# Optimization experiments

Measured on AMD Instinct MI355X. Metric: run time of the kernel, lower is better.

## Reference

```python
import jax, jax.numpy as jnp
import numpy as np

B, L, C, NH = 512, 196, 384, 12
HW = 14  # window side

def _relative_position_index(h, w):
    coords = np.stack(np.meshgrid(np.arange(h), np.arange(w), indexing='ij'))  # [2,h,w]
    cf = coords.reshape(2, -1)                       # [2, L]
    rel = cf[:, :, None] - cf[:, None, :]            # [2, L, L]
    rel = rel.transpose(1, 2, 0).astype(np.int64)    # [L, L, 2]
    rel[..., 0] += h - 1
    rel[..., 1] += w - 1
    rel[..., 0] *= 2 * w - 1
    return rel.sum(-1)                               # [L, L]

def setup_inputs() -> dict:
    key = jax.random.key(0)
    ks = jax.random.split(key, 5)
    hd = C // NH
    x = jax.random.normal(ks[0], (B, L, C), dtype=jnp.float32)
    # weights stored as [in, out] (equivalent to torch Linear weight.T)
    qkv_w = jax.random.normal(ks[1], (C, 3 * C), dtype=jnp.float32) * (C ** -0.5)
    qkv_b = jnp.zeros((3 * C,), dtype=jnp.float32)
    proj_w = jax.random.normal(ks[2], (C, C), dtype=jnp.float32) * (C ** -0.5)
    proj_b = jnp.zeros((C,), dtype=jnp.float32)
    bias_table = jax.random.normal(ks[3], ((2 * HW - 1) ** 2, NH), dtype=jnp.float32) * 0.02
    rel_index = jnp.asarray(_relative_position_index(HW, HW), dtype=jnp.int32)
    return {"x": x, "qkv_w": qkv_w, "qkv_b": qkv_b, "proj_w": proj_w,
            "proj_b": proj_b, "bias_table": bias_table, "rel_index": rel_index}

def reference(x, qkv_w, qkv_b, proj_w, proj_b, bias_table, rel_index):
    b, l, c = x.shape
    nh = bias_table.shape[1]
    hd = c // nh
    scale = hd ** -0.5
    qkv = (x @ qkv_w + qkv_b).reshape(b, l, 3, nh, hd).transpose(2, 0, 3, 1, 4)  # [3,B,nh,L,hd]
    q, k, v = qkv[0] * scale, qkv[1], qkv[2]
    attn = jnp.einsum('bhqd,bhkd->bhqk', q, k)                 # [B,nh,L,L]
    bias = bias_table[rel_index]                               # [L,L,nh]
    attn = attn + bias.transpose(2, 0, 1)[None]                # add [1,nh,L,L]
    attn = jax.nn.softmax(attn, axis=-1)
    out = jnp.einsum('bhqk,bhkd->bhqd', attn, v)               # [B,nh,L,hd]
    out = out.transpose(0, 2, 1, 3).reshape(b, l, c)
    return out @ proj_w + proj_b
```

## Files before the change

### kernel.cpp

```cpp
#include <hip/hip_runtime.h>
#include <hip/hip_bf16.h>
#include <stdint.h>

typedef __hip_bfloat16 bf16;
typedef __attribute__((ext_vector_type(8))) short frag8;
typedef __attribute__((ext_vector_type(4))) float floatx4;

#define B_WIN 512
#define L_TOK 196
#define C_DIM 384
#define NH    12
#define HD    32
#define QP    208
#define KPAD  224
#define VSTR  236
#define QSCALE 0.2550348555f

#if defined(__has_builtin)
#if __has_builtin(__builtin_amdgcn_exp2f)
#define EXP2(x) __builtin_amdgcn_exp2f(x)
#endif
#endif
#ifndef EXP2
#define EXP2(x) exp2f(x)
#endif

__device__ __forceinline__ void async_cp16(const void* g, void* l) {
  __builtin_amdgcn_global_load_lds(
      (const __attribute__((address_space(1))) unsigned int*)g,
      (__attribute__((address_space(3))) unsigned int*)l, 16, 0, 0);
}

__device__ __forceinline__ unsigned short f2bf_bits(float f) {
  bf16 b = __float2bfloat16(f);
  return *(unsigned short*)&b;
}

__device__ __forceinline__ float bfu2f(short u) {
  union { uint32_t i; float f; } c;
  c.i = ((uint32_t)(unsigned short)u) << 16;
  return c.f;
}

__global__ void cast_to_bf16(const float* __restrict__ src, bf16* __restrict__ dst) {
  int i = blockIdx.x * 256 + threadIdx.x;
  float4 v = ((const float4*)src)[i];
  ushort4 o;
  o.x = f2bf_bits(v.x); o.y = f2bf_bits(v.y);
  o.z = f2bf_bits(v.z); o.w = f2bf_bits(v.w);
  ((ushort4*)dst)[i] = o;
}

__global__ void transpose_cast(const float* __restrict__ src, bf16* __restrict__ dst,
                               int K, int N) {
  int idx = blockIdx.x * 256 + threadIdx.x;
  if (idx >= K * N) return;
  int k = idx / N, n = idx - k * N;
  dst[n * K + k] = __float2bfloat16(src[idx]);
}

__global__ void bias_fill(const float* __restrict__ table, const int* __restrict__ rel,
                          bf16* __restrict__ biasb) {
  int idx = blockIdx.x * 256 + threadIdx.x;
  int h = idx / (QP * KPAD);
  int rem = idx - h * (QP * KPAD);
  int q = rem / KPAD, r2 = rem - q * KPAD;
  int kk = r2 >> 5, quad = (r2 >> 3) & 3, i = r2 & 7;
  int k = kk * 32 + quad * 8 + ((i >= 4) ? 4 : 0) + (i & 3);
  float v;
  if (q >= L_TOK)      v = 0.f;
  else if (k >= L_TOK) v = -1e30f;
  else                 v = table[rel[q * L_TOK + k] * NH + h] * 1.4426950408889634f;
  biasb[idx] = __float2bfloat16(v);
}

__device__ __forceinline__ void storev(bf16* p, float v)  { *p = __float2bfloat16(v); }
__device__ __forceinline__ void storev(float* p, float v) { *p = v; }

template <typename OT>
__global__ __launch_bounds__(256) void gemm_bt(
    const bf16* __restrict__ A, const bf16* __restrict__ Bt,
    const float* __restrict__ bias, OT* __restrict__ C,
    int M, int N, int K, int lda, int qcols, int nbn, int panel) {
  __shared__ __align__(16) bf16 sA[3][128 * 32];
  __shared__ __align__(16) bf16 sB[3][128 * 32];
  const int tid = threadIdx.x;
  const int wave = tid >> 6, lane = tid & 63;
  const int SUPER = panel * nbn;
  const int bid = blockIdx.x;
  const int sb = bid / SUPER, rsp = bid - sb * SUPER;
  const long bm = (long)(sb * panel + rsp % panel) * 128;
  const long bn = (long)(rsp / panel) * 128;

  const int srow = wave * 32 + (lane >> 2);
  const int scol = (lane & 3) * 8;
  const bf16* gA = A + (bm + srow) * (long)lda + scol;
  const bf16* gB = Bt + (bn + srow) * (long)K + scol;

  floatx4 acc[4][4];
#pragma unroll
  for (int i = 0; i < 4; i++)
#pragma unroll
    for (int j = 0; j < 4; j++) acc[i][j] = (floatx4)(0.f);

  const int wr = (wave & 1) * 64;
  const int wc = (wave >> 1) * 64;
  const int nst = K >> 5;

#define STAGE(s, buf)                                                        \
  do {                                                                       \
    _Pragma("unroll")                                                        \
    for (int j = 0; j < 2; j++) {                                            \
      async_cp16(gA + (size_t)j * 16 * lda + (s) * 32,                       \
                 &sA[buf][(wave * 32 + j * 16) * 32]);                       \
      async_cp16(gB + (size_t)j * 16 * K + (s) * 32,                         \
                 &sB[buf][(wave * 32 + j * 16) * 32]);                       \
    }                                                                        \
  } while (0)

  STAGE(0, 0);
  STAGE(1, 1);
  asm volatile("s_waitcnt vmcnt(4)" ::: "memory");
  __builtin_amdgcn_s_barrier();

  int cur = 0;
  for (int t = 0; t < nst; ++t) {
    if (t + 2 < nst) {
      int nb = cur + 2; if (nb >= 3) nb -= 3;
      STAGE(t + 2, nb);
    }
    frag8 af[4], bfr[4];
#pragma unroll
    for (int mi = 0; mi < 4; mi++)
      af[mi] = *(const frag8*)&sA[cur][(wr + mi * 16 + (lane & 15)) * 32 + (lane >> 4) * 8];
#pragma unroll
    for (int ni = 0; ni < 4; ni++)
      bfr[ni] = *(const frag8*)&sB[cur][(wc + ni * 16 + (lane & 15)) * 32 + (lane >> 4) * 8];
#pragma unroll
    for (int mi = 0; mi < 4; mi++)
#pragma unroll
      for (int ni = 0; ni < 4; ni++)
        acc[mi][ni] = __builtin_amdgcn_mfma_f32_16x16x32_bf16(af[mi], bfr[ni], acc[mi][ni], 0, 0, 0);
    if (t + 1 < nst) {
      if (t + 2 < nst) asm volatile("s_waitcnt vmcnt(4)" ::: "memory");
      else             asm volatile("s_waitcnt vmcnt(0)" ::: "memory");
      __builtin_amdgcn_s_barrier();
    }
    cur = (cur == 2) ? 0 : cur + 1;
  }
#undef STAGE

#pragma unroll
  for (int ni = 0; ni < 4; ni++) {
    const long col = bn + wc + ni * 16 + (lane & 15);
    const float bv = bias[col];
#pragma unroll
    for (int mi = 0; mi < 4; mi++)
#pragma unroll
      for (int r = 0; r < 4; r++) {
        const long row = bm + wr + mi * 16 + (lane >> 4) * 4 + r;
        float val = acc[mi][ni][r] + bv;
        if (col < qcols) val *= QSCALE;
        storev(&C[row * N + col], val);
      }
  }
}

__global__ __launch_bounds__(256) void attn_win(
    bf16* __restrict__ qkv, const bf16* __restrict__ biasb) {
  __shared__ __align__(16) bf16 kL[KPAD * 32];
  __shared__ __align__(16) bf16 vT[HD * VSTR];
  const int b = blockIdx.x, h = blockIdx.y;
  const int tid = threadIdx.x, wave = tid >> 6, lane = tid & 63;
  bf16* base = qkv + (size_t)b * L_TOK * (3 * C_DIM);

  const int colb = lane & 15;
  const int quad = lane >> 4;
  const int rsub = quad * 4;
  const int kswz = (quad ^ ((colb >> 1) & 3)) * 8;

  const bf16* vbase = base + 2 * C_DIM + h * HD;
  const int r0a = tid >> 2, c8a = (tid & 3) * 8;
  const bf16* ga = vbase + (size_t)(2 * r0a) * (3 * C_DIM) + c8a;
  uint4 a0 = *(const uint4*)ga;
  uint4 a1 = *(const uint4*)(ga + 3 * C_DIM);
  const int i1 = tid + 256;
  const bool h1 = i1 < 392;
  const int r0b = h1 ? (i1 >> 2) : r0a, c8b = h1 ? (i1 & 3) * 8 : c8a;
  const bf16* gb = vbase + (size_t)(2 * r0b) * (3 * C_DIM) + c8b;
  uint4 b0 = make_uint4(0, 0, 0, 0), b1 = make_uint4(0, 0, 0, 0);
  if (h1) { b0 = *(const uint4*)gb; b1 = *(const uint4*)(gb + 3 * C_DIM); }

  for (int c = wave; c < 14; c += 4) {
    const int j = c * 16 + (lane >> 2);
    const int slot = lane & 3;
    const int t = j >> 4, qd = (j >> 2) & 3, rr = j & 3;
    int k = (t >> 1) * 32 + qd * 8 + (t & 1) * 4 + rr;
    if (k > L_TOK - 1) k = L_TOK - 1;
    const int sj = (j >> 1) & 3;
    const bf16* src = base + (size_t)k * (3 * C_DIM) + C_DIM + h * HD + ((slot ^ sj) * 8);
    async_cp16(src, &kL[c * 512]);
  }

  {
    ushort ea0[8], ea1[8];
    *(uint4*)ea0 = a0; *(uint4*)ea1 = a1;
#pragma unroll
    for (int e = 0; e < 8; e++) {
      uint32_t pack = (uint32_t)ea0[e] | ((uint32_t)ea1[e] << 16);
      *(uint32_t*)&vT[(c8a + e) * VSTR + 2 * r0a] = pack;
    }
    if (h1) {
      ushort eb0[8], eb1[8];
      *(uint4*)eb0 = b0; *(uint4*)eb1 = b1;
#pragma unroll
      for (int e = 0; e < 8; e++) {
        uint32_t pack = (uint32_t)eb0[e] | ((uint32_t)eb1[e] << 16);
        *(uint32_t*)&vT[(c8b + e) * VSTR + 2 * r0b] = pack;
      }
    }
  }
  for (int idx = tid; idx < HD * 14; idx += 256) {
    int d = idx / 14, pr = idx - d * 14;
    *(uint32_t*)&vT[d * VSTR + L_TOK + 2 * pr] = 0;
  }
  __syncthreads();

  const bf16* biasB = biasb + (size_t)h * QP * KPAD;

#pragma unroll
  for (int ii = 0; ii < 4; ii++) {
    const int rg = wave + 4 * ii;
    if (rg < 13) {
      const int row0 = rg * 16;
      int qrow = row0 + colb; if (qrow > L_TOK - 1) qrow = L_TOK - 1;
      const frag8 aq = *(const frag8*)(base + (size_t)qrow * (3 * C_DIM) + h * HD + quad * 8);
      const bf16* bRow = biasB + (size_t)(row0 + colb) * KPAD;

      floatx4 o0 = (floatx4)(0.f), o1 = (floatx4)(0.f);
      float lsum = 0.f;
#pragma unroll
      for (int kk = 0; kk < 7; kk++) {
        const frag8 k0 = *(const frag8*)&kL[((2 * kk) * 16 + colb) * 32 + kswz];
        const frag8 k1 = *(const frag8*)&kL[((2 * kk + 1) * 16 + colb) * 32 + kswz];
        floatx4 s0 = __builtin_amdgcn_mfma_f32_16x16x32_bf16(k0, aq, (floatx4)(0.f), 0, 0, 0);
        floatx4 s1 = __builtin_amdgcn_mfma_f32_16x16x32_bf16(k1, aq, (floatx4)(0.f), 0, 0, 0);
        const frag8 bb = *(const frag8*)&bRow[kk * 32 + quad * 8];
        frag8 ap;
#pragma unroll
        for (int e = 0; e < 4; e++) {
          float p = EXP2(s0[e] + bfu2f(bb[e]));
          lsum += p;
          ap[e] = (short)f2bf_bits(p);
        }
#pragma unroll
        for (int e = 0; e < 4; e++) {
          float p = EXP2(s1[e] + bfu2f(bb[4 + e]));
          lsum += p;
          ap[4 + e] = (short)f2bf_bits(p);
        }
        const frag8 bv0 = *(const frag8*)&vT[colb * VSTR + kk * 32 + quad * 8];
        const frag8 bv1 = *(const frag8*)&vT[(16 + colb) * VSTR + kk * 32 + quad * 8];
        o0 = __builtin_amdgcn_mfma_f32_16x16x32_bf16(ap, bv0, o0, 0, 0, 0);
        o1 = __builtin_amdgcn_mfma_f32_16x16x32_bf16(ap, bv1, o1, 0, 0, 0);
      }
      lsum += __shfl_xor(lsum, 16, 64);
      lsum += __shfl_xor(lsum, 32, 64);
      const float rl = 1.0f / lsum;
#pragma unroll
      for (int r = 0; r < 4; r++) {
        const float rn = __shfl(rl, rsub + r, 64);
        const int grow = row0 + rsub + r;
        if (grow < L_TOK) {
          base[(size_t)grow * (3 * C_DIM) + h * HD + colb] = __float2bfloat16(o0[r] * rn);
          base[(size_t)grow * (3 * C_DIM) + h * HD + 16 + colb] = __float2bfloat16(o1[r] * rn);
        }
      }
    }
  }
}

extern "C" void kernel_launch(void* const* d_in, const int* in_sizes, int n_in,
                              void* d_out, int out_size, void* d_ws, size_t ws_size,
                              hipStream_t stream) {
  const float* x      = (const float*)d_in[0];
  const float* qkv_w  = (const float*)d_in[1];
  const float* qkv_b  = (const float*)d_in[2];
  const float* proj_w = (const float*)d_in[3];
  const float* proj_b = (const float*)d_in[4];
  const float* btab   = (const float*)d_in[5];
  const int*   relidx = (const int*)d_in[6];
  float* out = (float*)d_out;

  const size_t M = (size_t)B_WIN * L_TOK;
  char* ws = (char*)d_ws;
  size_t off = 0;
  bf16*  qkv   = (bf16*)(ws + off);  off += M * 1152 * 2;
  bf16*  wT1   = (bf16*)(ws + off);  off += (size_t)1152 * 384 * 2;
  bf16*  wT2   = (bf16*)(ws + off);  off += (size_t)384 * 384 * 2;
  bf16*  biasb = (bf16*)(ws + off);  off += (size_t)NH * QP * KPAD * 2;

  bf16* xb = (ws_size >= off + M * C_DIM * sizeof(bf16))
                 ? (bf16*)(ws + off) : (bf16*)d_out;

  cast_to_bf16<<<(int)(M * C_DIM / 4 / 256), 256, 0, stream>>>(x, xb);
  transpose_cast<<<(384 * 1152 + 255) / 256, 256, 0, stream>>>(qkv_w, wT1, 384, 1152);
  transpose_cast<<<(384 * 384 + 255) / 256, 256, 0, stream>>>(proj_w, wT2, 384, 384);
  bias_fill<<<(NH * QP * KPAD) / 256, 256, 0, stream>>>(btab, relidx, biasb);

  gemm_bt<bf16><<<784 * 9, 256, 0, stream>>>(xb, wT1, qkv_b, qkv,
                                             (int)M, 1152, 384, 384, C_DIM, 9, 28);
  attn_win<<<dim3(B_WIN, NH), 256, 0, stream>>>(qkv, biasb);
  gemm_bt<float><<<784 * 3, 256, 0, stream>>>(qkv, wT2, proj_b, out,
                                              (int)M, 384, 384, 1152, 0, 3, 28);
}
```

Before: 602.4 us.

## Load GEMM A fragments directly from global into registers, keep B in LDS

The GEMM stops staging the A operand through shared memory. Each wave loads its A MFMA fragments straight from global memory into registers, one k-step ahead, while B keeps its 3-stage async LDS pipeline. K and the A leading dimension become compile-time constants so the k-loop fully unrolls. This removes half the LDS traffic and staging, and halves LDS use, which may raise occupancy. The cost is uncoalesced-ish 16-byte per-lane global loads for A, A rows shared by two waves are fetched twice, and more registers are held for the prefetched fragments.

After: 676.6 us. 1.12x slower.

```diff
diff --git a/kernel.cpp b/kernel.cpp
--- a/kernel.cpp
+++ b/kernel.cpp
@@ -14,6 +14,8 @@
 #define QP    208
 #define KPAD  224
 #define VSTR  236
+#define GK    384
+#define NST   12
 #define QSCALE 0.2550348555f
 
 #if defined(__has_builtin)
@@ -77,12 +79,11 @@
 __device__ __forceinline__ void storev(bf16* p, float v)  { *p = __float2bfloat16(v); }
 __device__ __forceinline__ void storev(float* p, float v) { *p = v; }
 
-template <typename OT>
+template <typename OT, int LDA>
 __global__ __launch_bounds__(256) void gemm_bt(
     const bf16* __restrict__ A, const bf16* __restrict__ Bt,
     const float* __restrict__ bias, OT* __restrict__ C,
-    int M, int N, int K, int lda, int qcols, int nbn, int panel) {
-  __shared__ __align__(16) bf16 sA[3][128 * 32];
+    int M, int N, int qcols, int nbn, int panel) {
   __shared__ __align__(16) bf16 sB[3][128 * 32];
   const int tid = threadIdx.x;
   const int wave = tid >> 6, lane = tid & 63;
@@ -92,73 +93,84 @@
   const long bm = (long)(sb * panel + rsp % panel) * 128;
   const long bn = (long)(rsp / panel) * 128;
 
+  const int colb = lane & 15;
+  const int quad = lane >> 4;
   const int srow = wave * 32 + (lane >> 2);
   const int scol = (lane & 3) * 8;
-  const bf16* gA = A + (bm + srow) * (long)lda + scol;
-  const bf16* gB = Bt + (bn + srow) * (long)K + scol;
-
-  floatx4 acc[4][4];
-#pragma unroll
-  for (int i = 0; i < 4; i++)
-#pragma unroll
-    for (int j = 0; j < 4; j++) acc[i][j] = (floatx4)(0.f);
+  const bf16* gB = Bt + (bn + srow) * (long)GK + scol;
 
   const int wr = (wave & 1) * 64;
   const int wc = (wave >> 1) * 64;
-  const int nst = K >> 5;
-
-#define STAGE(s, buf)                                                        \
+  const bf16* gAf = A + (bm + wr + colb) * (long)LDA + quad * 8;
+
+  floatx4 acc[4][4];
+#pragma unroll
+  for (int i = 0; i < 4; i++)
+#pragma unroll
+    for (int j = 0; j < 4; j++) acc[i][j] = (floatx4)(0.f);
+
+#define STAGEB(s, buf)                                                       \
   do {                                                                       \
     _Pragma("unroll")                                                        \
-    for (int j = 0; j < 2; j++) {                                            \
-      async_cp16(gA + (size_t)j * 16 * lda + (s) * 32,                       \
-                 &sA[buf][(wave * 32 + j * 16) * 32]);                       \
-      async_cp16(gB + (size_t)j * 16 * K + (s) * 32,                         \
+    for (int j = 0; j < 2; j++)                                              \
+      async_cp16(gB + (size_t)j * 16 * GK + (s) * 32,                        \
                  &sB[buf][(wave * 32 + j * 16) * 32]);                       \
-    }                                                                        \
   } while (0)
-
-  STAGE(0, 0);
-  STAGE(1, 1);
-  asm volatile("s_waitcnt vmcnt(4)" ::: "memory");
+#define LOADA(dst, s)                                                        \
+  do {                                                                       \
+    _Pragma("unroll")                                                        \
+    for (int mi = 0; mi < 4; mi++)                                           \
+      dst[mi] = *(const frag8*)(gAf + (size_t)mi * 16 * LDA + (s) * 32);     \
+  } while (0)
+
+  frag8 af[4], afn[4];
+  STAGEB(0, 0);
+  asm volatile("" ::: "memory");
+  LOADA(af, 0);
+  asm volatile("" ::: "memory");
+  STAGEB(1, 1);
+  asm volatile("s_waitcnt vmcnt(2)" ::: "memory");
   __builtin_amdgcn_s_barrier();
 
   int cur = 0;
-  for (int t = 0; t < nst; ++t) {
-    if (t + 2 < nst) {
-      int nb = cur + 2; if (nb >= 3) nb -= 3;
-      STAGE(t + 2, nb);
-    }
-    frag8 af[4], bfr[4];
-#pragma unroll
-    for (int mi = 0; mi < 4; mi++)
-      af[mi] = *(const frag8*)&sA[cur][(wr + mi * 16 + (lane & 15)) * 32 + (lane >> 4) * 8];
+#pragma unroll
+  for (int t = 0; t < NST; ++t) {
+    const int sa = (t + 1 < NST) ? t + 1 : NST - 1;
+    LOADA(afn, sa);
+    const int sb2 = (t + 2 < NST) ? t + 2 : NST - 1;
+    int nb = cur + 2; if (nb >= 3) nb -= 3;
+    STAGEB(sb2, nb);
+
+    frag8 bfr[4];
 #pragma unroll
     for (int ni = 0; ni < 4; ni++)
-      bfr[ni] = *(const frag8*)&sB[cur][(wc + ni * 16 + (lane & 15)) * 32 + (lane >> 4) * 8];
+      bfr[ni] = *(const frag8*)&sB[cur][(wc + ni * 16 + colb) * 32 + quad * 8];
 #pragma unroll
     for (int mi = 0; mi < 4; mi++)
 #pragma unroll
       for (int ni = 0; ni < 4; ni++)
         acc[mi][ni] = __builtin_amdgcn_mfma_f32_16x16x32_bf16(af[mi], bfr[ni], acc[mi][ni], 0, 0, 0);
-    if (t + 1 < nst) {
-      if (t + 2 < nst) asm volatile("s_waitcnt vmcnt(4)" ::: "memory");
-      else             asm volatile("s_waitcnt vmcnt(0)" ::: "memory");
+#pragma unroll
+    for (int mi = 0; mi < 4; mi++) af[mi] = afn[mi];
+
+    if (t + 1 < NST) {
+      asm volatile("s_waitcnt vmcnt(6)" ::: "memory");
       __builtin_amdgcn_s_barrier();
     }
     cur = (cur == 2) ? 0 : cur + 1;
   }
-#undef STAGE
+#undef STAGEB
+#undef LOADA
 
 #pragma unroll
   for (int ni = 0; ni < 4; ni++) {
-    const long col = bn + wc + ni * 16 + (lane & 15);
+    const long col = bn + wc + ni * 16 + colb;
     const float bv = bias[col];
 #pragma unroll
     for (int mi = 0; mi < 4; mi++)
 #pragma unroll
       for (int r = 0; r < 4; r++) {
-        const long row = bm + wr + mi * 16 + (lane >> 4) * 4 + r;
+        const long row = bm + wr + mi * 16 + quad * 4 + r;
         float val = acc[mi][ni][r] + bv;
         if (col < qcols) val *= QSCALE;
         storev(&C[row * N + col], val);
@@ -308,9 +320,9 @@
   transpose_cast<<<(384 * 384 + 255) / 256, 256, 0, stream>>>(proj_w, wT2, 384, 384);
   bias_fill<<<(NH * QP * KPAD) / 256, 256, 0, stream>>>(btab, relidx, biasb);
 
-  gemm_bt<bf16><<<784 * 9, 256, 0, stream>>>(xb, wT1, qkv_b, qkv,
-                                             (int)M, 1152, 384, 384, C_DIM, 9, 28);
+  gemm_bt<bf16, 384><<<784 * 9, 256, 0, stream>>>(xb, wT1, qkv_b, qkv,
+                                                  (int)M, 1152, C_DIM, 9, 28);
   attn_win<<<dim3(B_WIN, NH), 256, 0, stream>>>(qkv, biasb);
-  gemm_bt<float><<<784 * 3, 256, 0, stream>>>(qkv, wT2, proj_b, out,
-                                              (int)M, 384, 384, 1152, 0, 3, 28);
-}
+  gemm_bt<float, 1152><<<784 * 3, 256, 0, stream>>>(qkv, wT2, proj_b, out,
+                                                    (int)M, 384, 0, 3, 28);
+}
```
